# Performance work log

Measured on AMD Instinct MI355X. Metric: run time of the kernel, lower is better.

The kernel has to match this reference:

```python
import jax, jax.numpy as jnp
import numpy as np

EMBED_DIM = 128
NUM_SYMBOLS = 200000
B = 1024
K = 200
PROCESS_STEPS = 4


def setup_inputs() -> dict:
    key = jax.random.key(0)
    ks = jax.random.split(key, 10)
    D = EMBED_DIM
    emb = jax.random.normal(ks[0], (NUM_SYMBOLS + 1, D), jnp.float32) * 0.02
    emb = emb.at[NUM_SYMBOLS].set(0.0)  # padding_idx row
    return {
        "relations": jax.random.randint(ks[1], (B, K), 0, NUM_SYMBOLS),
        "entities": jax.random.randint(ks[2], (B, K), 0, NUM_SYMBOLS),
        "query": jax.random.randint(ks[3], (B,), 0, NUM_SYMBOLS),
        "symbol_emb": emb,
        "gcn_w_w": jax.random.normal(ks[4], (D, 2 * D), jnp.float32) / np.sqrt(2 * D).astype(np.float32),
        "gcn_w_b": jnp.zeros((D,), jnp.float32),
        "p1_w": jax.random.normal(ks[5], (2 * D, D), jnp.float32) / np.sqrt(D).astype(np.float32),
        "p1_b": jnp.zeros((2 * D,), jnp.float32),
        "p2_w": jax.random.normal(ks[6], (D, 2 * D), jnp.float32) / np.sqrt(2 * D).astype(np.float32),
        "p2_b": jnp.zeros((D,), jnp.float32),
        "ln_a": jnp.ones((D,), jnp.float32),
        "ln_b": jnp.zeros((D,), jnp.float32),
        "w_ih": jax.random.normal(ks[7], (8 * D, D), jnp.float32) * 0.05,
        "w_hh": jax.random.normal(ks[8], (8 * D, 2 * D), jnp.float32) * 0.05,
        "b_ih": jnp.zeros((8 * D,), jnp.float32),
        "b_hh": jnp.zeros((8 * D,), jnp.float32),
    }


def _layer_norm(z, a, b, eps=1e-3):
    # repo's LayerNormalization: (z - mu) / (std + eps) * a + b, unbiased std
    mu = jnp.mean(z, axis=-1, keepdims=True)
    sigma = jnp.std(z, axis=-1, ddof=1, keepdims=True)
    return (z - mu) / (sigma + eps) * a + b


def _forward(symbol_emb, gcn_w_w, gcn_w_b, p1_w, p1_b, p2_w, p2_b,
             ln_a, ln_b, w_ih, w_hh, b_ih, b_hh,
             relations, entities, query):
    D = symbol_emb.shape[1]
    # --- neighbor_encoder: gather -> concat -> linear -> neighbor sum -> tanh
    rel_e = symbol_emb[relations]                       # (B, K, D)
    ent_e = symbol_emb[entities]                        # (B, K, D)
    concat = jnp.concatenate([rel_e, ent_e], axis=-1)   # (B, K, 2D)
    out = jnp.einsum('bkf,df->bkd', concat, gcn_w_w) + gcn_w_b
    num_neighbors = jnp.asarray(relations.shape[0], out.dtype)  # code uses relations.size()[0]
    support = jnp.tanh(out.sum(axis=1) / num_neighbors)  # (B, D)
    # --- SupportEncoder: FFN with residual + layernorm (dropout off in eval)
    hidden = jax.nn.relu(support @ p1_w.T + p1_b)        # (B, 2D)
    support_g = _layer_norm(hidden @ p2_w.T + p2_b + support, ln_a, ln_b)
    # --- QueryEncoder: LSTMCell(D, 2D) process block with attention over support
    q = symbol_emb[query]                                # (B, D)
    bsz = q.shape[0]
    h_r = jnp.zeros((bsz, 2 * D), q.dtype)
    c = jnp.zeros((bsz, 2 * D), q.dtype)
    h_out = q
    for _ in range(PROCESS_STEPS):
        gates = q @ w_ih.T + b_ih + h_r @ w_hh.T + b_hh  # (B, 8D)
        i, f, g, o = jnp.split(gates, 4, axis=-1)
        c = jax.nn.sigmoid(f) * c + jax.nn.sigmoid(i) * jnp.tanh(g)
        h_ = jax.nn.sigmoid(o) * jnp.tanh(c)             # (B, 2D)
        h_out = q + h_[:, :D]                            # (B, D)
        attn = jax.nn.softmax(h_out @ support_g.T, axis=1)  # (B, B)
        r = attn @ support_g                             # (B, D)
        h_r = jnp.concatenate([h_out, r], axis=-1)       # (B, 2D)
    query_embeds = h_out
    # --- cosine similarity over dim=1
    cross = jnp.sum(query_embeds * support_g, axis=1)
    n1 = jnp.sum(query_embeds * query_embeds, axis=1)
    n2 = jnp.sum(support_g * support_g, axis=1)
    return cross / jnp.sqrt(n1 * n2)                     # (B,)


def reference(relations, entities, query, symbol_emb, gcn_w_w, gcn_w_b,
              p1_w, p1_b, p2_w, p2_b, ln_a, ln_b, w_ih, w_hh, b_ih, b_hh):
    return _forward(symbol_emb, gcn_w_w, gcn_w_b, p1_w, p1_b, p2_w, p2_b,
                    ln_a, ln_b, w_ih, w_hh, b_ih, b_hh,
                    relations, entities, query)
```

## Files before the change

kernel.cpp:

```cpp
#include <hip/hip_runtime.h>
#include <math.h>

#define D 128
#define B_SZ 1024
#define KNB 200
#define AWQ 136
#define AWG 264
#define HW 136
#define SCW 1028
#define PW 1048

typedef _Float16 half8 __attribute__((ext_vector_type(8)));
typedef _Float16 half4 __attribute__((ext_vector_type(4)));
typedef float floatx4 __attribute__((ext_vector_type(4)));

__device__ __forceinline__ float sigmoid_f(float x) { return 1.f / (1.f + __expf(-x)); }
__device__ __forceinline__ float tanh_fast(float x) { return 1.f - 2.f / (__expf(2.f * x) + 1.f); }

__global__ __launch_bounds__(256) void k_cvtw(
    const float* __restrict__ w_ih, const float* __restrict__ w_hh,
    _Float16* __restrict__ w16)
{
    const int i8 = (blockIdx.x * 256 + threadIdx.x) * 8;
    const float* src = (i8 < 131072) ? (w_ih + i8) : (w_hh + (i8 - 131072));
    float4 v0 = *(const float4*)src;
    float4 v1 = *(const float4*)(src + 4);
    half8 h;
    h[0] = (_Float16)v0.x; h[1] = (_Float16)v0.y; h[2] = (_Float16)v0.z; h[3] = (_Float16)v0.w;
    h[4] = (_Float16)v1.x; h[5] = (_Float16)v1.y; h[6] = (_Float16)v1.z; h[7] = (_Float16)v1.w;
    *(half8*)&w16[i8] = h;
}

__global__ __launch_bounds__(512) void k_support(
    const int* __restrict__ relations, const int* __restrict__ entities,
    const int* __restrict__ query, const float* __restrict__ emb,
    const float* __restrict__ gcn_w, const float* __restrict__ gcn_b,
    const float* __restrict__ p1_w, const float* __restrict__ p1_b,
    const float* __restrict__ p2_w, const float* __restrict__ p2_b,
    const float* __restrict__ ln_a, const float* __restrict__ ln_b,
    float* __restrict__ sg, _Float16* __restrict__ sgH, _Float16* __restrict__ sgT,
    float* __restrict__ qb, _Float16* __restrict__ qbH)
{
    __shared__ int idxs[2 * KNB];
    __shared__ __align__(16) float part[16][132];
    __shared__ __align__(16) float S[2 * D];
    __shared__ __align__(16) float sup[D];
    __shared__ __align__(16) float hid[2 * D];
    __shared__ __align__(16) float zv[D];
    __shared__ float red2[2];

    const int b = blockIdx.x;
    const int t = threadIdx.x;

    if (t < KNB) idxs[t] = relations[b * KNB + t];
    else if (t < 2 * KNB) idxs[t] = entities[b * KNB + (t - KNB)];
    __syncthreads();

    {
        const int g = t >> 5, c4 = (t & 31) * 4;
        const int* mi = &idxs[(g >> 3) * KNB];
        float4 a4 = make_float4(0.f, 0.f, 0.f, 0.f);
        #pragma unroll 5
        for (int k = (g & 7); k < KNB; k += 8) {
            float4 v = *(const float4*)&emb[(size_t)mi[k] * D + c4];
            a4.x += v.x; a4.y += v.y; a4.z += v.z; a4.w += v.w;
        }
        *(float4*)&part[g][c4] = a4;
    }
    __syncthreads();
    if (t < 2 * D) {
        const int half = t >> 7, c = t & 127;
        float s = 0.f;
        #pragma unroll
        for (int j = 0; j < 8; ++j) s += part[half * 8 + j][c];
        S[t] = s;
    }
    __syncthreads();

    if (t < D) {
        const float4* w4 = (const float4*)(gcn_w + t * 2 * D);
        float dot = 0.f;
        #pragma unroll 8
        for (int f = 0; f < 2 * D / 4; ++f) {
            float4 w = w4[f];
            float4 s = *(const float4*)&S[f * 4];
            dot += w.x * s.x + w.y * s.y + w.z * s.z + w.w * s.w;
        }
        float v = (dot + 200.f * gcn_b[t]) * (1.f / 1024.f);
        sup[t] = tanhf(v);
    }
    __syncthreads();

    if (t < 2 * D) {
        const float4* w4 = (const float4*)(p1_w + t * D);
        float dot = 0.f;
        #pragma unroll 8
        for (int f = 0; f < D / 4; ++f) {
            float4 w = w4[f];
            float4 s = *(const float4*)&sup[f * 4];
            dot += w.x * s.x + w.y * s.y + w.z * s.z + w.w * s.w;
        }
        float h = dot + p1_b[t];
        hid[t] = h > 0.f ? h : 0.f;
    }
    __syncthreads();

    if (t < D) {
        const float4* w4 = (const float4*)(p2_w + t * 2 * D);
        float dot = 0.f;
        #pragma unroll 8
        for (int f = 0; f < 2 * D / 4; ++f) {
            float4 w = w4[f];
            float4 s = *(const float4*)&hid[f * 4];
            dot += w.x * s.x + w.y * s.y + w.z * s.z + w.w * s.w;
        }
        zv[t] = dot + p2_b[t] + sup[t];
    }
    __syncthreads();

    if (t < 64) {
        float x0 = zv[t], x1 = zv[t + 64];
        float s = x0 + x1;
        for (int off = 32; off; off >>= 1) s += __shfl_down(s, off);
        float mu = __shfl(s, 0) * (1.f / 128.f);
        float d0 = x0 - mu, d1 = x1 - mu;
        float v = d0 * d0 + d1 * d1;
        for (int off = 32; off; off >>= 1) v += __shfl_down(v, off);
        v = __shfl(v, 0);
        if (t == 0) { red2[0] = mu; red2[1] = sqrtf(v * (1.f / 127.f)); }
    }
    __syncthreads();
    if (t < D) {
        float mu = red2[0], sigma = red2[1];
        float val = (zv[t] - mu) / (sigma + 1e-3f) * ln_a[t] + ln_b[t];
        sg[b * D + t] = val;
        sgH[b * D + t] = (_Float16)val;
        sgT[t * B_SZ + b] = (_Float16)val;
        float qv = emb[(size_t)query[b] * D + t];
        qb[b * D + t] = qv;
        qbH[b * D + t] = (_Float16)qv;
    }
}

__global__ __launch_bounds__(256) void k_gq(
    const _Float16* __restrict__ qbH, const _Float16* __restrict__ w16,
    const float* __restrict__ b_ih, const float* __restrict__ b_hh,
    const float* __restrict__ qb, float* __restrict__ gqB,
    float* __restrict__ cbuf, float* __restrict__ hout, _Float16* __restrict__ houtH)
{
    __shared__ _Float16 Ah[64 * AWQ];
    __shared__ _Float16 Bh[2][4][16][40];

    const int t = threadIdx.x;
    const int b0 = blockIdx.x * 64;
    const int n0 = blockIdx.y * 16;
    const int lane = t & 63, wv = t >> 6;
    const int m = lane & 15, quad = lane >> 4;

    {
        const int row = t >> 2, gr = b0 + row;
        #pragma unroll
        for (int i = 0; i < 4; ++i) {
            const int c = (t & 3) * 8 + i * 32;
            *(half8*)&Ah[row * AWQ + c] = *(const half8*)&qbH[gr * D + c];
        }
    }
    const int sg_g = t >> 6, sg_u = (t >> 2) & 15, sg_kq = (t & 3) * 8;
    auto stage_b = [&](int ks, int buf) {
        const int grow = sg_g * 256 + n0 + sg_u;
        *(half8*)&Bh[buf][sg_g][sg_u][sg_kq] = *(const half8*)&w16[grow * D + ks * 32 + sg_kq];
    };
    stage_b(0, 0);
    __syncthreads();

    floatx4 acc[4];
    #pragma unroll
    for (int g = 0; g < 4; ++g)
        #pragma unroll
        for (int i = 0; i < 4; ++i) acc[g][i] = 0.f;

    for (int ks = 0; ks < 4; ++ks) {
        if (ks + 1 < 4) stage_b(ks + 1, (ks + 1) & 1);
        half8 a = *(const half8*)&Ah[(wv * 16 + m) * AWQ + ks * 32 + quad * 8];
        #pragma unroll
        for (int g = 0; g < 4; ++g) {
            half8 bf = *(const half8*)&Bh[ks & 1][g][m][quad * 8];
            acc[g] = __builtin_amdgcn_mfma_f32_16x16x32_f16(a, bf, acc[g], 0, 0, 0);
        }
        __syncthreads();
    }

    const int unit = n0 + m;
    float bi[4];
    #pragma unroll
    for (int g = 0; g < 4; ++g) bi[g] = b_ih[g * 256 + unit] + b_hh[g * 256 + unit];
    #pragma unroll
    for (int rr = 0; rr < 4; ++rr) {
        const int b = b0 + wv * 16 + quad * 4 + rr;
        #pragma unroll
        for (int g = 0; g < 4; ++g) gqB[(size_t)b * 1024 + g * 256 + unit] = acc[g][rr];
        float gi = acc[0][rr] + bi[0];
        float gg = acc[2][rr] + bi[2];
        float go = acc[3][rr] + bi[3];
        float cn = sigmoid_f(gi) * tanh_fast(gg);
        cbuf[b * 256 + unit] = cn;
        if (n0 < D) {
            float ho = qb[b * D + unit] + sigmoid_f(go) * tanh_fast(cn);
            hout[b * D + unit] = ho;
            houtH[b * D + unit] = (_Float16)ho;
        }
    }
}

__global__ __launch_bounds__(1024) void k_attn(
    const _Float16* __restrict__ hH, const _Float16* __restrict__ sgH,
    const _Float16* __restrict__ sgT, _Float16* __restrict__ rH)
{
    __shared__ _Float16 Hh[16 * HW];
    __shared__ float    Sc[16 * SCW];
    __shared__ _Float16 P[16 * PW];
    __shared__ float    sinv[16];
    __shared__ float    rpar[2][16][132];

    const int t = threadIdx.x;
    const int wv = t >> 6, lane = t & 63;
    const int m = lane & 15, quad = lane >> 4;
    const int b0 = blockIdx.x * 16;

    if (t < 256) {
        const int row = t >> 4, c = (t & 15) * 8;
        *(half8*)&Hh[row * HW + c] = *(const half8*)&hH[(b0 + row) * D + c];
    }
    __syncthreads();

    {
        floatx4 a2[4];
        #pragma unroll
        for (int i = 0; i < 4; ++i)
            #pragma unroll
            for (int z = 0; z < 4; ++z) a2[i][z] = 0.f;
        #pragma unroll
        for (int ks = 0; ks < 4; ++ks) {
            half8 a = *(const half8*)&Hh[m * HW + ks * 32 + quad * 8];
            #pragma unroll
            for (int i = 0; i < 4; ++i) {
                const int j0 = (wv * 4 + i) * 16;
                half8 bf = *(const half8*)&sgH[(j0 + m) * D + ks * 32 + quad * 8];
                a2[i] = __builtin_amdgcn_mfma_f32_16x16x32_f16(a, bf, a2[i], 0, 0, 0);
            }
        }
        #pragma unroll
        for (int i = 0; i < 4; ++i) {
            const int j0 = (wv * 4 + i) * 16;
            #pragma unroll
            for (int rr = 0; rr < 4; ++rr)
                Sc[(quad * 4 + rr) * SCW + j0 + m] = a2[i][rr];
        }
    }
    __syncthreads();

    {
        const int row = wv;
        float vals[16];
        float mm = -1e30f;
        #pragma unroll
        for (int j = 0; j < 16; ++j) {
            vals[j] = Sc[row * SCW + lane + j * 64];
            mm = fmaxf(mm, vals[j]);
        }
        #pragma unroll
        for (int off = 32; off; off >>= 1) mm = fmaxf(mm, __shfl_down(mm, off));
        mm = __shfl(mm, 0);
        float ss = 0.f;
        #pragma unroll
        for (int j = 0; j < 16; ++j) {
            float e = __expf(vals[j] - mm);
            P[row * PW + lane + j * 64] = (_Float16)e;
            ss += e;
        }
        #pragma unroll
        for (int off = 32; off; off >>= 1) ss += __shfl_down(ss, off);
        if (lane == 0) sinv[row] = 1.f / ss;
    }
    __syncthreads();

    {
        const int nt = wv & 7, kh = wv >> 3;
        floatx4 a3;
        #pragma unroll
        for (int z = 0; z < 4; ++z) a3[z] = 0.f;
        #pragma unroll
        for (int ks = 0; ks < 16; ++ks) {
            const int kk = kh * 16 + ks;
            half8 a = *(const half8*)&P[m * PW + kk * 32 + quad * 8];
            half8 bf = *(const half8*)&sgT[(nt * 16 + m) * B_SZ + kk * 32 + quad * 8];
            a3 = __builtin_amdgcn_mfma_f32_16x16x32_f16(a, bf, a3, 0, 0, 0);
        }
        #pragma unroll
        for (int rr = 0; rr < 4; ++rr)
            rpar[kh][quad * 4 + rr][nt * 16 + m] = a3[rr];
    }
    __syncthreads();

    if (t < 2048) {
        const int e = t;
        const int row = e >> 7, col = e & 127;
        float v = (rpar[0][row][col] + rpar[1][row][col]) * sinv[row];
        rH[(b0 + row) * D + col] = (_Float16)v;
    }
    if (t >= 1024 - 1024 + 1024) {}
    {
        const int e = t + 1024;
        if (e < 2048) {
            const int row = e >> 7, col = e & 127;
            float v = (rpar[0][row][col] + rpar[1][row][col]) * sinv[row];
            rH[(b0 + row) * D + col] = (_Float16)v;
        }
    }
}

__global__ __launch_bounds__(256) void k_gates(
    const _Float16* __restrict__ hHin, const _Float16* __restrict__ rH,
    const _Float16* __restrict__ w16, const float* __restrict__ gqB,
    const float* __restrict__ b_ih, const float* __restrict__ b_hh,
    const float* __restrict__ qb, float* __restrict__ cbuf,
    float* __restrict__ hout, _Float16* __restrict__ hHout)
{
    __shared__ _Float16 Ah[64 * AWG];
    __shared__ _Float16 Bh[2][4][16][40];

    const int t = threadIdx.x;
    const int b0 = blockIdx.x * 64;
    const int n0 = blockIdx.y * 16;
    const int lane = t & 63, wv = t >> 6;
    const int m = lane & 15, quad = lane >> 4;

    {
        const int row = t >> 2, gr = b0 + row;
        #pragma unroll
        for (int i = 0; i < 8; ++i) {
            const int c = (t & 3) * 8 + i * 32;
            half8 h;
            if (c < 128) h = *(const half8*)&hHin[gr * D + c];
            else         h = *(const half8*)&rH[gr * D + (c - 128)];
            *(half8*)&Ah[row * AWG + c] = h;
        }
    }
    const int sg_g = t >> 6, sg_u = (t >> 2) & 15, sg_kq = (t & 3) * 8;
    auto stage_b = [&](int ks, int buf) {
        const int grow = sg_g * 256 + n0 + sg_u;
        *(half8*)&Bh[buf][sg_g][sg_u][sg_kq] =
            *(const half8*)&w16[131072 + grow * 256 + ks * 32 + sg_kq];
    };
    stage_b(0, 0);

    const int unit = n0 + m;
    floatx4 acc[4];
    #pragma unroll
    for (int rr = 0; rr < 4; ++rr) {
        const int b = b0 + wv * 16 + quad * 4 + rr;
        #pragma unroll
        for (int g = 0; g < 4; ++g) acc[g][rr] = gqB[(size_t)b * 1024 + g * 256 + unit];
    }
    __syncthreads();

    for (int ks = 0; ks < 8; ++ks) {
        if (ks + 1 < 8) stage_b(ks + 1, (ks + 1) & 1);
        half8 a = *(const half8*)&Ah[(wv * 16 + m) * AWG + ks * 32 + quad * 8];
        #pragma unroll
        for (int g = 0; g < 4; ++g) {
            half8 bf = *(const half8*)&Bh[ks & 1][g][m][quad * 8];
            acc[g] = __builtin_amdgcn_mfma_f32_16x16x32_f16(a, bf, acc[g], 0, 0, 0);
        }
        __syncthreads();
    }

    float bi[4];
    #pragma unroll
    for (int g = 0; g < 4; ++g) bi[g] = b_ih[g * 256 + unit] + b_hh[g * 256 + unit];
    #pragma unroll
    for (int rr = 0; rr < 4; ++rr) {
        const int b = b0 + wv * 16 + quad * 4 + rr;
        float gi = acc[0][rr] + bi[0];
        float gf = acc[1][rr] + bi[1];
        float gg = acc[2][rr] + bi[2];
        float go = acc[3][rr] + bi[3];
        float cold = cbuf[b * 256 + unit];
        float cn = sigmoid_f(gf) * cold + sigmoid_f(gi) * tanh_fast(gg);
        cbuf[b * 256 + unit] = cn;
        if (n0 < D) {
            float ho = qb[b * D + unit] + sigmoid_f(go) * tanh_fast(cn);
            hout[b * D + unit] = ho;
            hHout[b * D + unit] = (_Float16)ho;
        }
    }
}

__global__ __launch_bounds__(64) void k_cosine(
    const float* __restrict__ hout, const float* __restrict__ sg,
    float* __restrict__ out)
{
    const int b = blockIdx.x, t = threadIdx.x;
    float a0 = hout[b * D + t], a1 = hout[b * D + t + 64];
    float s0 = sg[b * D + t], s1 = sg[b * D + t + 64];
    float cr = a0 * s0 + a1 * s1;
    float n1 = a0 * a0 + a1 * a1;
    float n2 = s0 * s0 + s1 * s1;
    for (int off = 32; off; off >>= 1) {
        cr += __shfl_down(cr, off);
        n1 += __shfl_down(n1, off);
        n2 += __shfl_down(n2, off);
    }
    if (t == 0) out[b] = cr / sqrtf(n1 * n2);
}

extern "C" void kernel_launch(void* const* d_in, const int* in_sizes, int n_in,
                              void* d_out, int out_size, void* d_ws, size_t ws_size,
                              hipStream_t stream)
{
    const int*   relations = (const int*)d_in[0];
    const int*   entities  = (const int*)d_in[1];
    const int*   query     = (const int*)d_in[2];
    const float* emb       = (const float*)d_in[3];
    const float* gcn_w     = (const float*)d_in[4];
    const float* gcn_b     = (const float*)d_in[5];
    const float* p1_w      = (const float*)d_in[6];
    const float* p1_b      = (const float*)d_in[7];
    const float* p2_w      = (const float*)d_in[8];
    const float* p2_b      = (const float*)d_in[9];
    const float* ln_a      = (const float*)d_in[10];
    const float* ln_b      = (const float*)d_in[11];
    const float* w_ih      = (const float*)d_in[12];
    const float* w_hh      = (const float*)d_in[13];
    const float* b_ih      = (const float*)d_in[14];
    const float* b_hh      = (const float*)d_in[15];

    float* ws = (float*)d_ws;
    float*     sg   = ws;
    float*     qb   = ws + 131072;
    float*     hoF  = ws + 262144;
    float*     cb   = ws + 393216;
    float*     gqB  = ws + 655360;
    _Float16*  sgH  = (_Float16*)(ws + 1703936);
    _Float16*  sgT  = (_Float16*)(ws + 1769472);
    _Float16*  qbH  = (_Float16*)(ws + 1835008);
    _Float16*  hHA  = (_Float16*)(ws + 1900544);
    _Float16*  hHB  = (_Float16*)(ws + 1966080);
    _Float16*  rH   = (_Float16*)(ws + 2031616);
    _Float16*  w16  = (_Float16*)(ws + 2097152);

    k_cvtw<<<dim3(192), dim3(256), 0, stream>>>(w_ih, w_hh, w16);
    k_support<<<dim3(B_SZ), dim3(512), 0, stream>>>(
        relations, entities, query, emb, gcn_w, gcn_b,
        p1_w, p1_b, p2_w, p2_b, ln_a, ln_b, sg, sgH, sgT, qb, qbH);

    k_gq<<<dim3(16, 16), dim3(256), 0, stream>>>(
        qbH, w16, b_ih, b_hh, qb, gqB, cb, hoF, hHB);

    k_attn<<<dim3(64), dim3(1024), 0, stream>>>(hHB, sgH, sgT, rH);
    k_gates<<<dim3(16, 16), dim3(256), 0, stream>>>(
        hHB, rH, w16, gqB, b_ih, b_hh, qb, cb, hoF, hHA);
    k_attn<<<dim3(64), dim3(1024), 0, stream>>>(hHA, sgH, sgT, rH);
    k_gates<<<dim3(16, 16), dim3(256), 0, stream>>>(
        hHA, rH, w16, gqB, b_ih, b_hh, qb, cb, hoF, hHB);
    k_attn<<<dim3(64), dim3(1024), 0, stream>>>(hHB, sgH, sgT, rH);
    k_gates<<<dim3(16, 16), dim3(256), 0, stream>>>(
        hHB, rH, w16, gqB, b_ih, b_hh, qb, cb, hoF, hHA);

    k_cosine<<<dim3(B_SZ), dim3(64), 0, stream>>>(hoF, sg, (float*)d_out);
}
```

Measured before the change: 303.8 us.

## Fuse LSTM process steps, attention and cosine into one persistent kernel

Replaces the chain of k_gq, three k_attn/k_gates pairs and k_cosine with a single kernel where each 1024-thread block owns 16 queries. The cell state, query-gate partials and hidden state stay in registers and shared memory instead of round-tripping through global buffers. Softmax is computed directly from MFMA accumulators with cross-wave shared reductions, which removes the score staging buffer. The costs are only 64 blocks on the GPU and each block re-reading the full fp16 w_ih/w_hh weights from global memory without shared-memory staging.

```diff
diff --git a/kernel.cpp b/kernel.cpp
--- a/kernel.cpp
+++ b/kernel.cpp
@@ -4,14 +4,11 @@
 #define D 128
 #define B_SZ 1024
 #define KNB 200
-#define AWQ 136
-#define AWG 264
-#define HW 136
-#define SCW 1028
+#define AHW 264
+#define QHW 136
 #define PW 1048
 
 typedef _Float16 half8 __attribute__((ext_vector_type(8)));
-typedef _Float16 half4 __attribute__((ext_vector_type(4)));
 typedef float floatx4 __attribute__((ext_vector_type(4)));
 
 __device__ __forceinline__ float sigmoid_f(float x) { return 1.f / (1.f + __expf(-x)); }
@@ -142,98 +139,76 @@
     }
 }
 
-__global__ __launch_bounds__(256) void k_gq(
-    const _Float16* __restrict__ qbH, const _Float16* __restrict__ w16,
+__global__ __launch_bounds__(1024) void k_lstm(
+    const _Float16* __restrict__ qbH, const float* __restrict__ qb,
+    const _Float16* __restrict__ sgH, const _Float16* __restrict__ sgT,
+    const float* __restrict__ sg, const _Float16* __restrict__ w16,
     const float* __restrict__ b_ih, const float* __restrict__ b_hh,
-    const float* __restrict__ qb, float* __restrict__ gqB,
-    float* __restrict__ cbuf, float* __restrict__ hout, _Float16* __restrict__ houtH)
+    float* __restrict__ out)
 {
-    __shared__ _Float16 Ah[64 * AWQ];
-    __shared__ _Float16 Bh[2][4][16][40];
+    __shared__ _Float16 Ah[16 * AHW];
+    __shared__ _Float16 qH[16 * QHW];
+    __shared__ _Float16 P[16 * PW];
+    __shared__ float qF[16][132];
+    __shared__ float hF[16][132];
+    __shared__ float rpar[2][16][132];
+    __shared__ float pred[16][17];
+    __shared__ float mrow[16];
+    __shared__ float sinv[16];
 
     const int t = threadIdx.x;
-    const int b0 = blockIdx.x * 64;
-    const int n0 = blockIdx.y * 16;
-    const int lane = t & 63, wv = t >> 6;
+    const int w = t >> 6, lane = t & 63;
     const int m = lane & 15, quad = lane >> 4;
-
-    {
-        const int row = t >> 2, gr = b0 + row;
-        #pragma unroll
-        for (int i = 0; i < 4; ++i) {
-            const int c = (t & 3) * 8 + i * 32;
-            *(half8*)&Ah[row * AWQ + c] = *(const half8*)&qbH[gr * D + c];
-        }
-    }
-    const int sg_g = t >> 6, sg_u = (t >> 2) & 15, sg_kq = (t & 3) * 8;
-    auto stage_b = [&](int ks, int buf) {
-        const int grow = sg_g * 256 + n0 + sg_u;
-        *(half8*)&Bh[buf][sg_g][sg_u][sg_kq] = *(const half8*)&w16[grow * D + ks * 32 + sg_kq];
-    };
-    stage_b(0, 0);
-    __syncthreads();
-
-    floatx4 acc[4];
+    const int b0 = blockIdx.x * 16;
+    const int u = w * 16 + m;
+
+    if (t < 256) {
+        const int row = t >> 4, c = (t & 15) * 8;
+        *(half8*)&qH[row * QHW + c] = *(const half8*)&qbH[(b0 + row) * D + c];
+    }
+    if (t < 512) {
+        const int row = t >> 5, c = (t & 31) * 4;
+        *(float4*)&qF[row][c] = *(const float4*)&qb[(b0 + row) * D + c];
+    }
+    float bi[4];
+    #pragma unroll
+    for (int g = 0; g < 4; ++g) bi[g] = b_ih[g * 256 + u] + b_hh[g * 256 + u];
+    __syncthreads();
+
+    floatx4 gqr[4];
     #pragma unroll
     for (int g = 0; g < 4; ++g)
         #pragma unroll
-        for (int i = 0; i < 4; ++i) acc[g][i] = 0.f;
-
+        for (int z = 0; z < 4; ++z) gqr[g][z] = 0.f;
+    #pragma unroll
     for (int ks = 0; ks < 4; ++ks) {
-        if (ks + 1 < 4) stage_b(ks + 1, (ks + 1) & 1);
-        half8 a = *(const half8*)&Ah[(wv * 16 + m) * AWQ + ks * 32 + quad * 8];
+        half8 a = *(const half8*)&qH[m * QHW + ks * 32 + quad * 8];
         #pragma unroll
         for (int g = 0; g < 4; ++g) {
-            half8 bf = *(const half8*)&Bh[ks & 1][g][m][quad * 8];
-            acc[g] = __builtin_amdgcn_mfma_f32_16x16x32_f16(a, bf, acc[g], 0, 0, 0);
-        }
-        __syncthreads();
-    }
-
-    const int unit = n0 + m;
-    float bi[4];
-    #pragma unroll
-    for (int g = 0; g < 4; ++g) bi[g] = b_ih[g * 256 + unit] + b_hh[g * 256 + unit];
+            half8 bf = *(const half8*)&w16[(g * 256 + u) * D + ks * 32 + quad * 8];
+            gqr[g] = __builtin_amdgcn_mfma_f32_16x16x32_f16(a, bf, gqr[g], 0, 0, 0);
+        }
+    }
+
+    float creg[4];
     #pragma unroll
     for (int rr = 0; rr < 4; ++rr) {
-        const int b = b0 + wv * 16 + quad * 4 + rr;
-        #pragma unroll
-        for (int g = 0; g < 4; ++g) gqB[(size_t)b * 1024 + g * 256 + unit] = acc[g][rr];
-        float gi = acc[0][rr] + bi[0];
-        float gg = acc[2][rr] + bi[2];
-        float go = acc[3][rr] + bi[3];
+        float gi = gqr[0][rr] + bi[0];
+        float gg = gqr[2][rr] + bi[2];
+        float go = gqr[3][rr] + bi[3];
         float cn = sigmoid_f(gi) * tanh_fast(gg);
-        cbuf[b * 256 + unit] = cn;
-        if (n0 < D) {
-            float ho = qb[b * D + unit] + sigmoid_f(go) * tanh_fast(cn);
-            hout[b * D + unit] = ho;
-            houtH[b * D + unit] = (_Float16)ho;
-        }
-    }
-}
-
-__global__ __launch_bounds__(1024) void k_attn(
-    const _Float16* __restrict__ hH, const _Float16* __restrict__ sgH,
-    const _Float16* __restrict__ sgT, _Float16* __restrict__ rH)
-{
-    __shared__ _Float16 Hh[16 * HW];
-    __shared__ float    Sc[16 * SCW];
-    __shared__ _Float16 P[16 * PW];
-    __shared__ float    sinv[16];
-    __shared__ float    rpar[2][16][132];
-
-    const int t = threadIdx.x;
-    const int wv = t >> 6, lane = t & 63;
-    const int m = lane & 15, quad = lane >> 4;
-    const int b0 = blockIdx.x * 16;
-
-    if (t < 256) {
-        const int row = t >> 4, c = (t & 15) * 8;
-        *(half8*)&Hh[row * HW + c] = *(const half8*)&hH[(b0 + row) * D + c];
-    }
-    __syncthreads();
-
-    {
+        creg[rr] = cn;
+        if (w < 8) {
+            const int row = quad * 4 + rr;
+            float ho = qF[row][u] + sigmoid_f(go) * tanh_fast(cn);
+            Ah[row * AHW + u] = (_Float16)ho;
+            hF[row][u] = ho;
+        }
+    }
+    __syncthreads();
+
+    #pragma unroll 1
+    for (int s = 0; s < 3; ++s) {
         floatx4 a2[4];
         #pragma unroll
         for (int i = 0; i < 4; ++i)
@@ -241,177 +216,140 @@
             for (int z = 0; z < 4; ++z) a2[i][z] = 0.f;
         #pragma unroll
         for (int ks = 0; ks < 4; ++ks) {
-            half8 a = *(const half8*)&Hh[m * HW + ks * 32 + quad * 8];
+            half8 a = *(const half8*)&Ah[m * AHW + ks * 32 + quad * 8];
             #pragma unroll
             for (int i = 0; i < 4; ++i) {
-                const int j0 = (wv * 4 + i) * 16;
+                const int j0 = (w * 4 + i) * 16;
                 half8 bf = *(const half8*)&sgH[(j0 + m) * D + ks * 32 + quad * 8];
                 a2[i] = __builtin_amdgcn_mfma_f32_16x16x32_f16(a, bf, a2[i], 0, 0, 0);
             }
         }
+
+        float mloc[4];
+        #pragma unroll
+        for (int rr = 0; rr < 4; ++rr) {
+            mloc[rr] = fmaxf(fmaxf(a2[0][rr], a2[1][rr]), fmaxf(a2[2][rr], a2[3][rr]));
+        }
+        #pragma unroll
+        for (int off = 1; off <= 8; off <<= 1)
+            #pragma unroll
+            for (int rr = 0; rr < 4; ++rr)
+                mloc[rr] = fmaxf(mloc[rr], __shfl_xor(mloc[rr], off));
+        if (m == 0) {
+            #pragma unroll
+            for (int rr = 0; rr < 4; ++rr) pred[w][quad * 4 + rr] = mloc[rr];
+        }
+        __syncthreads();
+        if (t < 16) {
+            float mm = -1e30f;
+            #pragma unroll
+            for (int ww = 0; ww < 16; ++ww) mm = fmaxf(mm, pred[ww][t]);
+            mrow[t] = mm;
+        }
+        __syncthreads();
+
+        float sloc[4] = {0.f, 0.f, 0.f, 0.f};
         #pragma unroll
         for (int i = 0; i < 4; ++i) {
-            const int j0 = (wv * 4 + i) * 16;
+            const int col = (w * 4 + i) * 16 + m;
+            #pragma unroll
+            for (int rr = 0; rr < 4; ++rr) {
+                const int row = quad * 4 + rr;
+                float e = __expf(a2[i][rr] - mrow[row]);
+                P[row * PW + col] = (_Float16)e;
+                sloc[rr] += e;
+            }
+        }
+        #pragma unroll
+        for (int off = 1; off <= 8; off <<= 1)
             #pragma unroll
             for (int rr = 0; rr < 4; ++rr)
-                Sc[(quad * 4 + rr) * SCW + j0 + m] = a2[i][rr];
-        }
-    }
-    __syncthreads();
+                sloc[rr] += __shfl_xor(sloc[rr], off);
+        if (m == 0) {
+            #pragma unroll
+            for (int rr = 0; rr < 4; ++rr) pred[w][quad * 4 + rr] = sloc[rr];
+        }
+        __syncthreads();
+        if (t < 16) {
+            float ss = 0.f;
+            #pragma unroll
+            for (int ww = 0; ww < 16; ++ww) ss += pred[ww][t];
+            sinv[t] = 1.f / ss;
+        }
+
+        {
+            const int nt = w & 7, kh = w >> 3;
+            floatx4 a3;
+            #pragma unroll
+            for (int z = 0; z < 4; ++z) a3[z] = 0.f;
+            #pragma unroll
+            for (int ks = 0; ks < 16; ++ks) {
+                const int kk = kh * 16 + ks;
+                half8 a = *(const half8*)&P[m * PW + kk * 32 + quad * 8];
+                half8 bf = *(const half8*)&sgT[(nt * 16 + m) * B_SZ + kk * 32 + quad * 8];
+                a3 = __builtin_amdgcn_mfma_f32_16x16x32_f16(a, bf, a3, 0, 0, 0);
+            }
+            #pragma unroll
+            for (int rr = 0; rr < 4; ++rr)
+                rpar[kh][quad * 4 + rr][nt * 16 + m] = a3[rr];
+        }
+        __syncthreads();
+
+        #pragma unroll
+        for (int half2 = 0; half2 < 2; ++half2) {
+            const int e = t + half2 * 1024;
+            const int row = e >> 7, dd = e & 127;
+            float v = (rpar[0][row][dd] + rpar[1][row][dd]) * sinv[row];
+            Ah[row * AHW + 128 + dd] = (_Float16)v;
+        }
+        __syncthreads();
+
+        floatx4 acc[4];
+        #pragma unroll
+        for (int g = 0; g < 4; ++g) acc[g] = gqr[g];
+        #pragma unroll
+        for (int ks = 0; ks < 8; ++ks) {
+            half8 a = *(const half8*)&Ah[m * AHW + ks * 32 + quad * 8];
+            #pragma unroll
+            for (int g = 0; g < 4; ++g) {
+                half8 bf = *(const half8*)&w16[131072 + (g * 256 + u) * 256 + ks * 32 + quad * 8];
+                acc[g] = __builtin_amdgcn_mfma_f32_16x16x32_f16(a, bf, acc[g], 0, 0, 0);
+            }
+        }
+        __syncthreads();
+
+        #pragma unroll
+        for (int rr = 0; rr < 4; ++rr) {
+            float gi = acc[0][rr] + bi[0];
+            float gf = acc[1][rr] + bi[1];
+            float gg = acc[2][rr] + bi[2];
+            float go = acc[3][rr] + bi[3];
+            float cn = sigmoid_f(gf) * creg[rr] + sigmoid_f(gi) * tanh_fast(gg);
+            creg[rr] = cn;
+            if (w < 8) {
+                const int row = quad * 4 + rr;
+                float ho = qF[row][u] + sigmoid_f(go) * tanh_fast(cn);
+                Ah[row * AHW + u] = (_Float16)ho;
+                hF[row][u] = ho;
+            }
+        }
+        __syncthreads();
+    }
 
     {
-        const int row = wv;
-        float vals[16];
-        float mm = -1e30f;
-        #pragma unroll
-        for (int j = 0; j < 16; ++j) {
-            vals[j] = Sc[row * SCW + lane + j * 64];
-            mm = fmaxf(mm, vals[j]);
-        }
-        #pragma unroll
-        for (int off = 32; off; off >>= 1) mm = fmaxf(mm, __shfl_down(mm, off));
-        mm = __shfl(mm, 0);
-        float ss = 0.f;
-        #pragma unroll
-        for (int j = 0; j < 16; ++j) {
-            float e = __expf(vals[j] - mm);
-            P[row * PW + lane + j * 64] = (_Float16)e;
-            ss += e;
-        }
-        #pragma unroll
-        for (int off = 32; off; off >>= 1) ss += __shfl_down(ss, off);
-        if (lane == 0) sinv[row] = 1.f / ss;
-    }
-    __syncthreads();
-
-    {
-        const int nt = wv & 7, kh = wv >> 3;
-        floatx4 a3;
-        #pragma unroll
-        for (int z = 0; z < 4; ++z) a3[z] = 0.f;
-        #pragma unroll
-        for (int ks = 0; ks < 16; ++ks) {
-            const int kk = kh * 16 + ks;
-            half8 a = *(const half8*)&P[m * PW + kk * 32 + quad * 8];
-            half8 bf = *(const half8*)&sgT[(nt * 16 + m) * B_SZ + kk * 32 + quad * 8];
-            a3 = __builtin_amdgcn_mfma_f32_16x16x32_f16(a, bf, a3, 0, 0, 0);
-        }
-        #pragma unroll
-        for (int rr = 0; rr < 4; ++rr)
-            rpar[kh][quad * 4 + rr][nt * 16 + m] = a3[rr];
-    }
-    __syncthreads();
-
-    if (t < 2048) {
-        const int e = t;
-        const int row = e >> 7, col = e & 127;
-        float v = (rpar[0][row][col] + rpar[1][row][col]) * sinv[row];
-        rH[(b0 + row) * D + col] = (_Float16)v;
-    }
-    if (t >= 1024 - 1024 + 1024) {}
-    {
-        const int e = t + 1024;
-        if (e < 2048) {
-            const int row = e >> 7, col = e & 127;
-            float v = (rpar[0][row][col] + rpar[1][row][col]) * sinv[row];
-            rH[(b0 + row) * D + col] = (_Float16)v;
-        }
-    }
-}
-
-__global__ __launch_bounds__(256) void k_gates(
-    const _Float16* __restrict__ hHin, const _Float16* __restrict__ rH,
-    const _Float16* __restrict__ w16, const float* __restrict__ gqB,
-    const float* __restrict__ b_ih, const float* __restrict__ b_hh,
-    const float* __restrict__ qb, float* __restrict__ cbuf,
-    float* __restrict__ hout, _Float16* __restrict__ hHout)
-{
-    __shared__ _Float16 Ah[64 * AWG];
-    __shared__ _Float16 Bh[2][4][16][40];
-
-    const int t = threadIdx.x;
-    const int b0 = blockIdx.x * 64;
-    const int n0 = blockIdx.y * 16;
-    const int lane = t & 63, wv = t >> 6;
-    const int m = lane & 15, quad = lane >> 4;
-
-    {
-        const int row = t >> 2, gr = b0 + row;
-        #pragma unroll
-        for (int i = 0; i < 8; ++i) {
-            const int c = (t & 3) * 8 + i * 32;
-            half8 h;
-            if (c < 128) h = *(const half8*)&hHin[gr * D + c];
-            else         h = *(const half8*)&rH[gr * D + (c - 128)];
-            *(half8*)&Ah[row * AWG + c] = h;
-        }
-    }
-    const int sg_g = t >> 6, sg_u = (t >> 2) & 15, sg_kq = (t & 3) * 8;
-    auto stage_b = [&](int ks, int buf) {
-        const int grow = sg_g * 256 + n0 + sg_u;
-        *(half8*)&Bh[buf][sg_g][sg_u][sg_kq] =
-            *(const half8*)&w16[131072 + grow * 256 + ks * 32 + sg_kq];
-    };
-    stage_b(0, 0);
-
-    const int unit = n0 + m;
-    floatx4 acc[4];
-    #pragma unroll
-    for (int rr = 0; rr < 4; ++rr) {
-        const int b = b0 + wv * 16 + quad * 4 + rr;
-        #pragma unroll
-        for (int g = 0; g < 4; ++g) acc[g][rr] = gqB[(size_t)b * 1024 + g * 256 + unit];
-    }
-    __syncthreads();
-
-    for (int ks = 0; ks < 8; ++ks) {
-        if (ks + 1 < 8) stage_b(ks + 1, (ks + 1) & 1);
-        half8 a = *(const half8*)&Ah[(wv * 16 + m) * AWG + ks * 32 + quad * 8];
-        #pragma unroll
-        for (int g = 0; g < 4; ++g) {
-            half8 bf = *(const half8*)&Bh[ks & 1][g][m][quad * 8];
-            acc[g] = __builtin_amdgcn_mfma_f32_16x16x32_f16(a, bf, acc[g], 0, 0, 0);
-        }
-        __syncthreads();
-    }
-
-    float bi[4];
-    #pragma unroll
-    for (int g = 0; g < 4; ++g) bi[g] = b_ih[g * 256 + unit] + b_hh[g * 256 + unit];
-    #pragma unroll
-    for (int rr = 0; rr < 4; ++rr) {
-        const int b = b0 + wv * 16 + quad * 4 + rr;
-        float gi = acc[0][rr] + bi[0];
-        float gf = acc[1][rr] + bi[1];
-        float gg = acc[2][rr] + bi[2];
-        float go = acc[3][rr] + bi[3];
-        float cold = cbuf[b * 256 + unit];
-        float cn = sigmoid_f(gf) * cold + sigmoid_f(gi) * tanh_fast(gg);
-        cbuf[b * 256 + unit] = cn;
-        if (n0 < D) {
-            float ho = qb[b * D + unit] + sigmoid_f(go) * tanh_fast(cn);
-            hout[b * D + unit] = ho;
-            hHout[b * D + unit] = (_Float16)ho;
-        }
-    }
-}
-
-__global__ __launch_bounds__(64) void k_cosine(
-    const float* __restrict__ hout, const float* __restrict__ sg,
-    float* __restrict__ out)
-{
-    const int b = blockIdx.x, t = threadIdx.x;
-    float a0 = hout[b * D + t], a1 = hout[b * D + t + 64];
-    float s0 = sg[b * D + t], s1 = sg[b * D + t + 64];
-    float cr = a0 * s0 + a1 * s1;
-    float n1 = a0 * a0 + a1 * a1;
-    float n2 = s0 * s0 + s1 * s1;
-    for (int off = 32; off; off >>= 1) {
-        cr += __shfl_down(cr, off);
-        n1 += __shfl_down(n1, off);
-        n2 += __shfl_down(n2, off);
-    }
-    if (t == 0) out[b] = cr / sqrtf(n1 * n2);
+        const int row = w;
+        float a0 = hF[row][lane], a1 = hF[row][lane + 64];
+        float s0 = sg[(b0 + row) * D + lane], s1 = sg[(b0 + row) * D + lane + 64];
+        float cr = a0 * s0 + a1 * s1;
+        float n1 = a0 * a0 + a1 * a1;
+        float n2 = s0 * s0 + s1 * s1;
+        for (int off = 32; off; off >>= 1) {
+            cr += __shfl_down(cr, off);
+            n1 += __shfl_down(n1, off);
+            n2 += __shfl_down(n2, off);
+        }
+        if (lane == 0) out[b0 + row] = cr / sqrtf(n1 * n2);
+    }
 }
 
 extern "C" void kernel_launch(void* const* d_in, const int* in_sizes, int n_in,
@@ -438,34 +376,15 @@
     float* ws = (float*)d_ws;
     float*     sg   = ws;
     float*     qb   = ws + 131072;
-    float*     hoF  = ws + 262144;
-    float*     cb   = ws + 393216;
-    float*     gqB  = ws + 655360;
-    _Float16*  sgH  = (_Float16*)(ws + 1703936);
-    _Float16*  sgT  = (_Float16*)(ws + 1769472);
-    _Float16*  qbH  = (_Float16*)(ws + 1835008);
-    _Float16*  hHA  = (_Float16*)(ws + 1900544);
-    _Float16*  hHB  = (_Float16*)(ws + 1966080);
-    _Float16*  rH   = (_Float16*)(ws + 2031616);
-    _Float16*  w16  = (_Float16*)(ws + 2097152);
+    _Float16*  sgH  = (_Float16*)(ws + 262144);
+    _Float16*  sgT  = (_Float16*)(ws + 327680);
+    _Float16*  qbH  = (_Float16*)(ws + 393216);
+    _Float16*  w16  = (_Float16*)(ws + 458752);
 
     k_cvtw<<<dim3(192), dim3(256), 0, stream>>>(w_ih, w_hh, w16);
     k_support<<<dim3(B_SZ), dim3(512), 0, stream>>>(
         relations, entities, query, emb, gcn_w, gcn_b,
         p1_w, p1_b, p2_w, p2_b, ln_a, ln_b, sg, sgH, sgT, qb, qbH);
-
-    k_gq<<<dim3(16, 16), dim3(256), 0, stream>>>(
-        qbH, w16, b_ih, b_hh, qb, gqB, cb, hoF, hHB);
-
-    k_attn<<<dim3(64), dim3(1024), 0, stream>>>(hHB, sgH, sgT, rH);
-    k_gates<<<dim3(16, 16), dim3(256), 0, stream>>>(
-        hHB, rH, w16, gqB, b_ih, b_hh, qb, cb, hoF, hHA);
-    k_attn<<<dim3(64), dim3(1024), 0, stream>>>(hHA, sgH, sgT, rH);
-    k_gates<<<dim3(16, 16), dim3(256), 0, stream>>>(
-        hHA, rH, w16, gqB, b_ih, b_hh, qb, cb, hoF, hHB);
-    k_attn<<<dim3(64), dim3(1024), 0, stream>>>(hHB, sgH, sgT, rH);
-    k_gates<<<dim3(16, 16), dim3(256), 0, stream>>>(
-        hHB, rH, w16, gqB, b_ih, b_hh, qb, cb, hoF, hHA);
-
-    k_cosine<<<dim3(B_SZ), dim3(64), 0, stream>>>(hoF, sg, (float*)d_out);
+    k_lstm<<<dim3(64), dim3(1024), 0, stream>>>(
+        qbH, qb, sgH, sgT, sg, w16, b_ih, b_hh, (float*)d_out);
 }
```

Result: slower. 377.1 us (+24.1%).
